# Performance work log

Measured on AMD Instinct MI355X. Metric: run time of the kernel, lower is better.

Reference implementation:

```python
import jax, jax.numpy as jnp
import numpy as np

K = 3          # kernel_size
EPS = 1e-5     # BatchNorm eps


def setup_inputs() -> dict:
    key = jax.random.key(0)
    k1, k2, k3 = jax.random.split(key, 3)
    n, C, H, W = 8, 64, 128, 128
    x = jax.random.normal(k1, (n, C, H, W), dtype=jnp.float32)
    conv_w = jax.random.normal(k2, (C * K * K, C), dtype=jnp.float32) * np.sqrt(2.0 / (C * K * K))
    bn_gamma = jnp.ones((C * K * K,), dtype=jnp.float32)
    bn_beta = jnp.zeros((C * K * K,), dtype=jnp.float32)
    bn_mean = jnp.zeros((C * K * K,), dtype=jnp.float32)
    bn_var = jax.random.uniform(k3, (C * K * K,), dtype=jnp.float32)
    return {"x": x, "conv_w": conv_w, "bn_gamma": bn_gamma, "bn_beta": bn_beta,
            "bn_mean": bn_mean, "bn_var": bn_var}


def reference(x, conv_w, bn_gamma, bn_beta, bn_mean, bn_var):
    n, C, H, W = x.shape
    # ---- per-image dynamic filter: GAP -> 1x1 conv -> BN (eval) -> softmax over k^2 ----
    f = x.mean(axis=(2, 3))                       # (n, C)
    f = f @ conv_w.T                              # (n, C*9)  (1x1 conv on 1x1 map, no bias)
    f = (f - bn_mean) * (bn_gamma / jnp.sqrt(bn_var + EPS)) + bn_beta
    f = jax.nn.softmax(f.reshape(n, C, K * K), axis=-1)   # softmax over kernel positions
    # ---- reflect-pad + unfold (im2col), row-major kernel offsets matching F.unfold ----
    xp = jnp.pad(x, ((0, 0), (0, 0), (1, 1), (1, 1)), mode="reflect")
    patches = jnp.stack([xp[:, :, i:i + H, j:j + W]
                         for i in range(K) for j in range(K)], axis=2)  # (n, C, 9, H, W)
    # ---- softmax-weighted dynamic sum over the 9 taps ----
    out = jnp.einsum("nckhw,nck->nchw", patches, f)
    return out, x - out
```

## Files before the change

kernel.cpp:

```cpp
#include <hip/hip_runtime.h>

#define WW 128
#define HWSZ 16384
#define CC 64
#define NPLANE 512
#define NCHW 8388608
#define BN_EPS 1e-5f

typedef float v4f __attribute__((ext_vector_type(4)));

__global__ __launch_bounds__(256) void dc_mean_kernel(const float* __restrict__ x,
                                                      float* __restrict__ means) {
    const int plane = blockIdx.x;
    const v4f* xp = (const v4f*)(x + (size_t)plane * HWSZ);
    float s = 0.f;
#pragma unroll
    for (int i = 0; i < 16; ++i) {
        v4f v = xp[threadIdx.x + i * 256];
        s += v.x + v.y + v.z + v.w;
    }
    for (int off = 32; off > 0; off >>= 1)
        s += __shfl_down(s, off, 64);
    __shared__ float wsum[4];
    if ((threadIdx.x & 63) == 0) wsum[threadIdx.x >> 6] = s;
    __syncthreads();
    if (threadIdx.x == 0)
        means[plane] = (wsum[0] + wsum[1] + wsum[2] + wsum[3]) * (1.0f / 16384.0f);
}

__global__ __launch_bounds__(256) void dc_conv_kernel(const float* __restrict__ x,
                                                      const float* __restrict__ means,
                                                      const float* __restrict__ conv_w,
                                                      const float* __restrict__ gamma,
                                                      const float* __restrict__ beta,
                                                      const float* __restrict__ bn_mean,
                                                      const float* __restrict__ bn_var,
                                                      float* __restrict__ out) {
    const int plane = blockIdx.x >> 1;
    const int band  = blockIdx.x & 1;
    const int tid   = threadIdx.x;
    const int n = plane >> 6;
    const int c = plane & 63;

    __shared__ float lv[9];
    if (tid < 144) {
        const int j    = tid >> 4;
        const int part = tid & 15;
        const int jj = c * 9 + j;
        v4f mv = *(const v4f*)(means + n * CC + part * 4);
        v4f wv = *(const v4f*)(conv_w + (size_t)jj * CC + part * 4);
        float d = mv.x * wv.x + mv.y * wv.y + mv.z * wv.z + mv.w * wv.w;
        d += __shfl_down(d, 8, 16);
        d += __shfl_down(d, 4, 16);
        d += __shfl_down(d, 2, 16);
        d += __shfl_down(d, 1, 16);
        if (part == 0) {
            const float g = gamma[jj] * rsqrtf(bn_var[jj] + BN_EPS);
            lv[j] = (d - bn_mean[jj]) * g + beta[jj];
        }
    }
    __syncthreads();

    float w9[9];
    {
        float m = lv[0];
#pragma unroll
        for (int t = 1; t < 9; ++t) m = fmaxf(m, lv[t]);
        float den = 0.f;
        float e[9];
#pragma unroll
        for (int t = 0; t < 9; ++t) { e[t] = __expf(lv[t] - m); den += e[t]; }
        const float inv = 1.0f / den;
#pragma unroll
        for (int t = 0; t < 9; ++t) w9[t] = e[t] * inv;
    }

    const int g  = tid >> 5;
    const int q  = tid & 31;
    const int w0 = q * 4;
    const int r0 = band * 64 + g * 8;
    const float* xpl = x + (size_t)plane * HWSZ;

    v4f cP, cC, cN, cX;
    float eP0, eP1, eC0, eC1, eN0, eN1, eX0, eX1;

#define LOADROW(R, c4, e0, e1)                                              \
    {                                                                       \
        int RR = ((R) < 0) ? 1 : (((R) > 127) ? 126 : (R));                 \
        c4 = *(const v4f*)(xpl + RR * WW + w0);                             \
        float lft = __shfl_up(c4.w, 1, 32);                                 \
        float rgt = __shfl_down(c4.x, 1, 32);                               \
        e0 = (w0 == 0)   ? c4.y : lft;           \
        e1 = (w0 == 124) ? c4.z : rgt;          \
    }

    LOADROW(r0 - 1, cP, eP0, eP1);
    LOADROW(r0,     cC, eC0, eC1);
    LOADROW(r0 + 1, cN, eN0, eN1);

#pragma unroll
    for (int i = 0; i < 8; ++i) {
        const int h = r0 + i;
        if (i < 7) { LOADROW(h + 2, cX, eX0, eX1); }

        const float VP[6] = {eP0, cP.x, cP.y, cP.z, cP.w, eP1};
        const float VC[6] = {eC0, cC.x, cC.y, cC.z, cC.w, eC1};
        const float VN[6] = {eN0, cN.x, cN.y, cN.z, cN.w, eN1};

        float o[4];
#pragma unroll
        for (int p = 0; p < 4; ++p) {
            float acc = 0.f;
#pragma unroll
            for (int t = 0; t < 3; ++t) {
                acc = fmaf(w9[t],     VP[p + t], acc);
                acc = fmaf(w9[3 + t], VC[p + t], acc);
                acc = fmaf(w9[6 + t], VN[p + t], acc);
            }
            o[p] = acc;
        }

        const size_t base = (size_t)plane * HWSZ + (size_t)h * WW + w0;
        v4f ov = {o[0], o[1], o[2], o[3]};
        v4f dv = {cC.x - o[0], cC.y - o[1], cC.z - o[2], cC.w - o[3]};
        __builtin_nontemporal_store(ov, (v4f*)(out + base));
        __builtin_nontemporal_store(dv, (v4f*)(out + NCHW + base));

        cP = cC; eP0 = eC0; eP1 = eC1;
        cC = cN; eC0 = eN0; eC1 = eN1;
        cN = cX; eN0 = eX0; eN1 = eX1;
    }
#undef LOADROW
}

extern "C" void kernel_launch(void* const* d_in, const int* in_sizes, int n_in,
                              void* d_out, int out_size, void* d_ws, size_t ws_size,
                              hipStream_t stream) {
    const float* x       = (const float*)d_in[0];
    const float* conv_w  = (const float*)d_in[1];
    const float* gamma   = (const float*)d_in[2];
    const float* beta    = (const float*)d_in[3];
    const float* bn_mean = (const float*)d_in[4];
    const float* bn_var  = (const float*)d_in[5];
    float* out = (float*)d_out;
    float* means = (float*)d_ws;

    dc_mean_kernel<<<NPLANE, 256, 0, stream>>>(x, means);
    dc_conv_kernel<<<NPLANE * 2, 256, 0, stream>>>(x, means, conv_w, gamma, beta,
                                                   bn_mean, bn_var, out);
}
```

Baseline: 108.3 us.

## Fuse mean and dynamic conv into one kernel with per-image grid barrier

Replaces the separate mean and conv kernels with one fused kernel. Each block stages a 32-row band plus halo rows in LDS and computes a partial sum. The partials are exchanged through global memory, with a per-image atomic counter acting as a spin barrier. The conv then reads from LDS, so x is read from DRAM once instead of twice. The cost is a spin-wait that needs all 2048 blocks to be co-resident (256 per image) to avoid deadlock, plus an extra memset launch.

```diff
diff --git a/kernel.cpp b/kernel.cpp
--- a/kernel.cpp
+++ b/kernel.cpp
@@ -9,45 +9,77 @@
 
 typedef float v4f __attribute__((ext_vector_type(4)));
 
-__global__ __launch_bounds__(256) void dc_mean_kernel(const float* __restrict__ x,
-                                                      float* __restrict__ means) {
-    const int plane = blockIdx.x;
-    const v4f* xp = (const v4f*)(x + (size_t)plane * HWSZ);
+__global__ __launch_bounds__(256, 8) void dc_fused_kernel(
+    const float* __restrict__ x,
+    const float* __restrict__ conv_w,
+    const float* __restrict__ gamma,
+    const float* __restrict__ beta,
+    const float* __restrict__ bn_mean,
+    const float* __restrict__ bn_var,
+    float* __restrict__ out,
+    float* __restrict__ partial,
+    int* __restrict__ cnt)
+{
+    __shared__ __align__(16) float tile[34 * WW];
+    __shared__ float smean[CC];
+    __shared__ float lv[9];
+    __shared__ float wsum[4];
+
+    const int blk   = blockIdx.x;
+    const int plane = blk >> 2;
+    const int band  = blk & 3;
+    const int n = plane >> 6;
+    const int c = plane & 63;
+    const int b0 = band * 32;
+    const int tid = threadIdx.x;
+    const float* xpl = x + (size_t)plane * HWSZ;
+
+    const v4f* src = (const v4f*)(xpl + (size_t)b0 * WW);
     float s = 0.f;
 #pragma unroll
-    for (int i = 0; i < 16; ++i) {
-        v4f v = xp[threadIdx.x + i * 256];
+    for (int i = 0; i < 4; ++i) {
+        const int idx = tid + i * 256;
+        v4f v = src[idx];
+        ((v4f*)tile)[idx] = v;
         s += v.x + v.y + v.z + v.w;
+    }
+    if (tid < 64) {
+        const int hr   = (tid < 32) ? (b0 - 1) : (b0 + 32);
+        const int slot = (tid < 32) ? 32 : 33;
+        const int q    = tid & 31;
+        const int RR = (hr < 0) ? 1 : ((hr > 127) ? 126 : hr);
+        v4f v = *(const v4f*)(xpl + (size_t)RR * WW + q * 4);
+        ((v4f*)tile)[slot * 32 + q] = v;
     }
     for (int off = 32; off > 0; off >>= 1)
         s += __shfl_down(s, off, 64);
-    __shared__ float wsum[4];
-    if ((threadIdx.x & 63) == 0) wsum[threadIdx.x >> 6] = s;
+    if ((tid & 63) == 0) wsum[tid >> 6] = s;
     __syncthreads();
-    if (threadIdx.x == 0)
-        means[plane] = (wsum[0] + wsum[1] + wsum[2] + wsum[3]) * (1.0f / 16384.0f);
-}
 
-__global__ __launch_bounds__(256) void dc_conv_kernel(const float* __restrict__ x,
-                                                      const float* __restrict__ means,
-                                                      const float* __restrict__ conv_w,
-                                                      const float* __restrict__ gamma,
-                                                      const float* __restrict__ beta,
-                                                      const float* __restrict__ bn_mean,
-                                                      const float* __restrict__ bn_var,
-                                                      float* __restrict__ out) {
-    const int plane = blockIdx.x >> 1;
-    const int band  = blockIdx.x & 1;
-    const int tid   = threadIdx.x;
-    const int n = plane >> 6;
-    const int c = plane & 63;
+    if (tid == 0) {
+        const float tot = wsum[0] + wsum[1] + wsum[2] + wsum[3];
+        __hip_atomic_store(&partial[plane * 4 + band], tot,
+                           __ATOMIC_RELAXED, __HIP_MEMORY_SCOPE_AGENT);
+        __hip_atomic_fetch_add(&cnt[n], 1, __ATOMIC_RELEASE, __HIP_MEMORY_SCOPE_AGENT);
+        while (__hip_atomic_load(&cnt[n], __ATOMIC_ACQUIRE, __HIP_MEMORY_SCOPE_AGENT) < 256)
+            __builtin_amdgcn_s_sleep(1);
+    }
+    __syncthreads();
 
-    __shared__ float lv[9];
+    if (tid < CC) {
+        const float* pp = partial + n * 256 + tid * 4;
+        float t0 = __hip_atomic_load(pp + 0, __ATOMIC_RELAXED, __HIP_MEMORY_SCOPE_AGENT);
+        float t1 = __hip_atomic_load(pp + 1, __ATOMIC_RELAXED, __HIP_MEMORY_SCOPE_AGENT);
+        float t2 = __hip_atomic_load(pp + 2, __ATOMIC_RELAXED, __HIP_MEMORY_SCOPE_AGENT);
+        float t3 = __hip_atomic_load(pp + 3, __ATOMIC_RELAXED, __HIP_MEMORY_SCOPE_AGENT);
+        smean[tid] = (t0 + t1 + t2 + t3) * (1.0f / 16384.0f);
+    }
+    __syncthreads();
     if (tid < 144) {
         const int j    = tid >> 4;
         const int part = tid & 15;
         const int jj = c * 9 + j;
-        v4f mv = *(const v4f*)(means + n * CC + part * 4);
+        v4f mv = *(const v4f*)(smean + part * 4);
         v4f wv = *(const v4f*)(conv_w + (size_t)jj * CC + part * 4);
         float d = mv.x * wv.x + mv.y * wv.y + mv.z * wv.z + mv.w * wv.w;
         d += __shfl_down(d, 8, 16);
@@ -78,30 +110,23 @@
     const int g  = tid >> 5;
     const int q  = tid & 31;
     const int w0 = q * 4;
-    const int r0 = band * 64 + g * 8;
-    const float* xpl = x + (size_t)plane * HWSZ;
-
-    v4f cP, cC, cN, cX;
-    float eP0, eP1, eC0, eC1, eN0, eN1, eX0, eX1;
-
-#define LOADROW(R, c4, e0, e1)                                              \
-    {                                                                       \
-        int RR = ((R) < 0) ? 1 : (((R) > 127) ? 126 : (R));                 \
-        c4 = *(const v4f*)(xpl + RR * WW + w0);                             \
-        float lft = __shfl_up(c4.w, 1, 32);                                 \
-        float rgt = __shfl_down(c4.x, 1, 32);                               \
-        e0 = (w0 == 0)   ? c4.y : lft;           \
-        e1 = (w0 == 124) ? c4.z : rgt;          \
-    }
-
-    LOADROW(r0 - 1, cP, eP0, eP1);
-    LOADROW(r0,     cC, eC0, eC1);
-    LOADROW(r0 + 1, cN, eN0, eN1);
 
 #pragma unroll
-    for (int i = 0; i < 8; ++i) {
-        const int h = r0 + i;
-        if (i < 7) { LOADROW(h + 2, cX, eX0, eX1); }
+    for (int i = 0; i < 4; ++i) {
+        const int h = b0 + g * 4 + i;
+        const int sP = (h == b0)      ? 32 : (h - 1 - b0);
+        const int sC = h - b0;
+        const int sN = (h == b0 + 31) ? 33 : (h + 1 - b0);
+
+        v4f cP = ((const v4f*)tile)[sP * 32 + q];
+        v4f cC = ((const v4f*)tile)[sC * 32 + q];
+        v4f cN = ((const v4f*)tile)[sN * 32 + q];
+
+        float eP0 = __shfl_up(cP.w, 1, 32), eP1 = __shfl_down(cP.x, 1, 32);
+        float eC0 = __shfl_up(cC.w, 1, 32), eC1 = __shfl_down(cC.x, 1, 32);
+        float eN0 = __shfl_up(cN.w, 1, 32), eN1 = __shfl_down(cN.x, 1, 32);
+        if (w0 == 0)   { eP0 = cP.y; eC0 = cC.y; eN0 = cN.y; }
+        if (w0 == 124) { eP1 = cP.z; eC1 = cC.z; eN1 = cN.z; }
 
         const float VP[6] = {eP0, cP.x, cP.y, cP.z, cP.w, eP1};
         const float VC[6] = {eC0, cC.x, cC.y, cC.z, cC.w, eC1};
@@ -122,15 +147,10 @@
 
         const size_t base = (size_t)plane * HWSZ + (size_t)h * WW + w0;
         v4f ov = {o[0], o[1], o[2], o[3]};
-        v4f dv = {cC.x - o[0], cC.y - o[1], cC.z - o[2], cC.w - o[3]};
+        v4f dv = {VC[1] - o[0], VC[2] - o[1], VC[3] - o[2], VC[4] - o[3]};
         __builtin_nontemporal_store(ov, (v4f*)(out + base));
         __builtin_nontemporal_store(dv, (v4f*)(out + NCHW + base));
-
-        cP = cC; eP0 = eC0; eP1 = eC1;
-        cC = cN; eC0 = eN0; eC1 = eN1;
-        cN = cX; eN0 = eX0; eN1 = eX1;
     }
-#undef LOADROW
 }
 
 extern "C" void kernel_launch(void* const* d_in, const int* in_sizes, int n_in,
@@ -143,9 +163,12 @@
     const float* bn_mean = (const float*)d_in[4];
     const float* bn_var  = (const float*)d_in[5];
     float* out = (float*)d_out;
-    float* means = (float*)d_ws;
 
-    dc_mean_kernel<<<NPLANE, 256, 0, stream>>>(x, means);
-    dc_conv_kernel<<<NPLANE * 2, 256, 0, stream>>>(x, means, conv_w, gamma, beta,
-                                                   bn_mean, bn_var, out);
+    int*   cnt     = (int*)d_ws;
+    float* partial = (float*)((char*)d_ws + 128);
+
+    hipMemsetAsync(cnt, 0, 8 * sizeof(int), stream);
+    dc_fused_kernel<<<NPLANE * 4, 256, 0, stream>>>(x, conv_w, gamma, beta,
+                                                    bn_mean, bn_var, out,
+                                                    partial, cnt);
 }
```

New measurement: 284.1 us. 162% more time.
